# Performance work log

Measured on AMD Instinct MI355X. Metric: run time of the kernel, lower is better.

## Reference

```python
import jax, jax.numpy as jnp
import numpy as np

N = 65536          # nodes
E = 1048576        # edges (avg degree 16)
K = 5              # B-spline kernel size per dim (dim=3 -> 125 kernels)
F_IN, F_OUT = 1, 32
GRID = 32          # first sparse_voxel_max_pool: size = 1/32 -> 32^3 voxels
NUM_VOX = GRID ** 3

# enumerate the 2^3 corners of the degree-1 B-spline support
_BITS = np.array([[(b >> d) & 1 for d in range(3)] for b in range(8)], dtype=np.int32)  # [8,3]
_STRIDES = np.array([1, K, K * K], dtype=np.int32)  # kernel index strides per dim


def setup_inputs() -> dict:
    key = jax.random.key(0)
    ks = jax.random.split(key, 7)
    x = jax.random.normal(ks[0], (N, F_IN), dtype=jnp.float32)
    edge_index = jax.random.randint(ks[1], (2, E), 0, N, dtype=jnp.int32)
    pseudo = jax.random.uniform(ks[2], (E, 3), dtype=jnp.float32)   # edge pseudo-coords in [0,1]^3
    pos = jax.random.uniform(ks[3], (N, 3), dtype=jnp.float32)      # node positions in [0,1]^3
    W = jax.random.normal(ks[4], (K ** 3, F_IN, F_OUT), dtype=jnp.float32) * 0.1
    W_root = jax.random.normal(ks[5], (F_IN, F_OUT), dtype=jnp.float32) * 0.1
    bias = jax.random.normal(ks[6], (F_OUT,), dtype=jnp.float32) * 0.1
    return {"x": x, "edge_index": edge_index, "pseudo": pseudo, "pos": pos,
            "W": W, "W_root": W_root, "bias": bias}


def spline_basis(pseudo):
    """Degree-1 open B-spline basis. Returns (weights [E,8], kernel_idx [E,8])."""
    v = pseudo * (K - 1)                                   # [E,3] in [0, K-1]
    i0 = jnp.clip(jnp.floor(v), 0, K - 2)                  # lower knot per dim
    f = v - i0                                             # fractional part
    i0 = i0.astype(jnp.int32)
    bits = jnp.asarray(_BITS)                              # [8,3]
    idx = i0[:, None, :] + bits[None]                      # [E,8,3]
    w = jnp.where(bits[None].astype(bool), f[:, None, :], 1.0 - f[:, None, :])
    B = w.prod(axis=-1)                                    # [E,8]
    kidx = (idx * jnp.asarray(_STRIDES)).sum(axis=-1)      # [E,8] in [0,125)
    return B, kidx


def spline_conv(x, edge_index, pseudo, W, W_root, bias):
    src, dst = edge_index[0], edge_index[1]
    B, kidx = spline_basis(pseudo)                         # [E,8], [E,8]
    xj = x[src]                                            # [E,F_IN] edge-wise gather
    Wg = W[kidx]                                           # [E,8,F_IN,F_OUT]
    msg = jnp.einsum('es,ef,esfo->eo', B, xj, Wg)          # basis-weighted messages [E,F_OUT]
    agg = jax.ops.segment_sum(msg, dst, num_segments=N)    # scatter-add
    deg = jax.ops.segment_sum(jnp.ones((E,), jnp.float32), dst, num_segments=N)
    out = agg / jnp.clip(deg, 1.0)[:, None] + x @ W_root + bias  # mean aggr + root + bias
    return out


def reference(x, edge_index, pseudo, pos, W, W_root, bias):
    h = jax.nn.elu(spline_conv(x, edge_index, pseudo, W, W_root, bias))  # [N,32]
    # sparse voxel max pooling: hash positions to a 32^3 grid, scatter-max features
    vid = jnp.clip(jnp.floor(pos * GRID), 0, GRID - 1).astype(jnp.int32)  # [N,3]
    vidx = vid[:, 0] + GRID * vid[:, 1] + GRID * GRID * vid[:, 2]         # [N]
    pooled = jax.ops.segment_max(h, vidx, num_segments=NUM_VOX)           # [32768,32]
    pooled = jnp.where(jnp.isfinite(pooled), pooled, 0.0)                 # empty voxels -> 0
    return pooled
```

## Files before the change

kernel.cpp:

```cpp
#include <hip/hip_runtime.h>
#include <math.h>

#define F_OUT     32
#define GRID_DIM  32
#define NUM_VOX   (GRID_DIM * GRID_DIM * GRID_DIM)

#define NPB   64
#define NBKT  1024
#define SEB   2048
#define SCS   132
#define DEGS  125
#define ECAP  3072

__device__ __forceinline__ unsigned int enc_f32(float f) {
    unsigned int u = __float_as_uint(f);
    return (u & 0x80000000u) ? ~u : (u | 0x80000000u);
}
__device__ __forceinline__ float dec_f32(unsigned int e) {
    return (e & 0x80000000u) ? __uint_as_float(e ^ 0x80000000u)
                             : __uint_as_float(~e);
}

__global__ __launch_bounds__(512, 4) void sort_kernel(
    const int*   __restrict__ src,
    const int*   __restrict__ dst,
    const float* __restrict__ x,
    const float* __restrict__ pseudo,
    float4* __restrict__ payload,
    unsigned int* __restrict__ off_tab,
    int E)
{
    __shared__ unsigned int sHist[NBKT];
    __shared__ unsigned int sStart[NBKT];
    __shared__ unsigned int sWTot[8];
    __shared__ __align__(16) float4 sPay[SEB];

    const int t    = threadIdx.x;
    const int lane = t & 63;
    const int wv   = t >> 6;
    const int e0   = blockIdx.x * SEB;

    for (int i = t; i < NBKT; i += 512) sHist[i] = 0;
    __syncthreads();

    unsigned short dloc[4];
    float4 pay[4];
    #pragma unroll
    for (int i = 0; i < 4; ++i) {
        int e = e0 + i * 512 + t;
        if (e < E) {
            int d = dst[e];
            int s = src[e];
            float p0 = pseudo[3 * e], p1 = pseudo[3 * e + 1], p2 = pseudo[3 * e + 2];
            float xj = x[s];
            unsigned int q2 = (unsigned int)(p2 * 65535.0f + 0.5f) & 0xFFFFu;
            unsigned int w  = q2 | ((unsigned int)(d & 63) << 16);
            dloc[i] = (unsigned short)d;
            pay[i]  = make_float4(p0, p1, xj, __uint_as_float(w));
            atomicAdd(&sHist[d >> 6], 1u);
        } else dloc[i] = 0;
    }
    __syncthreads();

    unsigned int a0 = sHist[2 * t], a1 = sHist[2 * t + 1];
    unsigned int pairSum = a0 + a1;
    unsigned int incl = pairSum;
    #pragma unroll
    for (int d = 1; d < 64; d <<= 1) {
        unsigned int v = __shfl_up(incl, d, 64);
        if (lane >= d) incl += v;
    }
    if (lane == 63) sWTot[wv] = incl;
    __syncthreads();
    unsigned int wofs = 0, total = 0;
    #pragma unroll
    for (int w = 0; w < 8; ++w) {
        unsigned int v = sWTot[w];
        if (w < wv) wofs += v;
        total += v;
    }
    unsigned int ex = wofs + incl - pairSum;
    sStart[2 * t]     = ex;
    sStart[2 * t + 1] = ex + a0;
    sHist[2 * t]      = ex;
    sHist[2 * t + 1]  = ex + a0;
    __syncthreads();

    #pragma unroll
    for (int i = 0; i < 4; ++i) {
        int e = e0 + i * 512 + t;
        if (e < E) {
            unsigned int slot = atomicAdd(&sHist[dloc[i] >> 6], 1u);
            sPay[slot] = pay[i];
        }
    }
    __syncthreads();

    for (unsigned int i = t; i < total; i += 512)
        payload[(size_t)e0 + i] = sPay[i];

    for (int b = t; b < NBKT; b += 512) {
        unsigned int s = sStart[b];
        unsigned int nxt = (b < NBKT - 1) ? sStart[b + 1] : total;
        off_tab[(size_t)blockIdx.x * NBKT + b] = s | ((nxt - s) << 16);
    }
}

__device__ __forceinline__ void process_edge(float4 r, float* sC)
{
    float xj = r.z;
    unsigned int w = __float_as_uint(r.w);
    int   rel = (int)((w >> 16) & 63u);
    float p2  = (float)(w & 0xFFFFu) * (1.0f / 65535.0f);

    float v0 = r.x * 4.0f, v1 = r.y * 4.0f, v2 = p2 * 4.0f;
    float i0 = fminf(fmaxf(floorf(v0), 0.0f), 3.0f);
    float i1 = fminf(fmaxf(floorf(v1), 0.0f), 3.0f);
    float i2 = fminf(fmaxf(floorf(v2), 0.0f), 3.0f);
    float f0 = v0 - i0, f1 = v1 - i1, f2 = v2 - i2;
    float g0 = 1.0f - f0, g1 = 1.0f - f1, g2 = 1.0f - f2;
    int k = (int)i0 + 5 * (int)i1 + 25 * (int)i2;

    float w00 = g0 * g1, w10 = f0 * g1, w01 = g0 * f1, w11 = f0 * f1;
    float a2 = xj * g2, b2 = xj * f2;
    float* row = sC + rel * SCS;
    atomicAdd(row + k +  0, w00 * a2);
    atomicAdd(row + k +  1, w10 * a2);
    atomicAdd(row + k +  5, w01 * a2);
    atomicAdd(row + k +  6, w11 * a2);
    atomicAdd(row + k + 25, w00 * b2);
    atomicAdd(row + k + 26, w10 * b2);
    atomicAdd(row + k + 30, w01 * b2);
    atomicAdd(row + k + 31, w11 * b2);
    atomicAdd(row + DEGS, 1.0f);
}

__global__ __launch_bounds__(512) void owner_kernel(
    const float4* __restrict__ payload,
    const unsigned int* __restrict__ off_tab,
    const float* __restrict__ W,
    const float* __restrict__ x,
    const float* __restrict__ W_root,
    const float* __restrict__ bias,
    float4* __restrict__ h4,
    int Nn, int nSB)
{
    __shared__ __align__(16) float sC[NPB * SCS];
    __shared__ unsigned int sEdge[ECAP];
    __shared__ unsigned int sNe;

    const int t = threadIdx.x;
    const int b = blockIdx.x;
    const int lane = t & 63;

    for (int i = t; i < NPB * SCS / 4; i += 512)
        *(float4*)&sC[i * 4] = make_float4(0.f, 0.f, 0.f, 0.f);
    if (t == 0) sNe = 0;

    unsigned int cnt = 0, start_g = 0;
    if (t < nSB) {
        unsigned int packed = off_tab[(size_t)t * NBKT + b];
        start_g = (unsigned int)t * SEB + (packed & 0xFFFFu);
        cnt = packed >> 16;
    }
    __syncthreads();

    unsigned int incl = cnt;
    #pragma unroll
    for (int d = 1; d < 64; d <<= 1) {
        unsigned int v = __shfl_up(incl, d, 64);
        if (lane >= d) incl += v;
    }
    unsigned int wtot = __shfl(incl, 63, 64);
    unsigned int wbase = 0;
    if (lane == 63 && wtot > 0) wbase = atomicAdd(&sNe, wtot);
    wbase = __shfl(wbase, 63, 64);
    unsigned int off = wbase + incl - cnt;

    for (unsigned int j = 0; j < cnt; ++j) {
        unsigned int p = off + j;
        if (p < ECAP) sEdge[p] = start_g + j;
        else process_edge(payload[start_g + j], sC);
    }
    __syncthreads();

    int ne = (int)sNe; if (ne > ECAP) ne = ECAP;
    for (int i = t; i < ne; i += 512)
        process_edge(payload[sEdge[i]], sC);
    __syncthreads();

    const int node = t & 63;
    const int cg   = t >> 6;
    const float* crow = sC + node * SCS;
    float4 acc = make_float4(0.f, 0.f, 0.f, 0.f);
    #pragma unroll 8
    for (int k4 = 0; k4 < 31; ++k4) {
        float4 r = *(const float4*)&crow[k4 * 4];
        const float* wp = W + (k4 * 4) * F_OUT + cg * 4;
        float4 w0 = *(const float4*)(wp);
        float4 w1 = *(const float4*)(wp + F_OUT);
        float4 w2 = *(const float4*)(wp + 2 * F_OUT);
        float4 w3 = *(const float4*)(wp + 3 * F_OUT);
        acc.x += r.x * w0.x + r.y * w1.x + r.z * w2.x + r.w * w3.x;
        acc.y += r.x * w0.y + r.y * w1.y + r.z * w2.y + r.w * w3.y;
        acc.z += r.x * w0.z + r.y * w1.z + r.z * w2.z + r.w * w3.z;
        acc.w += r.x * w0.w + r.y * w1.w + r.z * w2.w + r.w * w3.w;
    }
    {
        float r = crow[124];
        const float* wp = W + 124 * F_OUT + cg * 4;
        acc.x += r * wp[0]; acc.y += r * wp[1];
        acc.z += r * wp[2]; acc.w += r * wp[3];
    }
    float dg = fmaxf(crow[DEGS], 1.0f);
    int   n  = b * NPB + node;
    float xn = (n < Nn) ? x[n] : 0.0f;
    float4 wr = *(const float4*)(W_root + cg * 4);
    float4 bs = *(const float4*)(bias + cg * 4);
    __syncthreads();

    if (n < Nn) {
        float h;
        h = acc.x / dg + xn * wr.x + bs.x; h = h > 0.f ? h : expm1f(h); sC[node * SCS + cg * 4 + 0] = h;
        h = acc.y / dg + xn * wr.y + bs.y; h = h > 0.f ? h : expm1f(h); sC[node * SCS + cg * 4 + 1] = h;
        h = acc.z / dg + xn * wr.z + bs.z; h = h > 0.f ? h : expm1f(h); sC[node * SCS + cg * 4 + 2] = h;
        h = acc.w / dg + xn * wr.w + bs.w; h = h > 0.f ? h : expm1f(h); sC[node * SCS + cg * 4 + 3] = h;
    }
    __syncthreads();

    const int n0 = b * NPB;
    for (int item = t; item < NPB * 8; item += 512) {
        int nr = item >> 3, q = item & 7;
        if (n0 + nr >= Nn) break;
        h4[(size_t)n0 * 8 + item] = *(const float4*)&sC[nr * SCS + q * 4];
    }
}

__global__ __launch_bounds__(256) void voxmax_kernel(
    const float* __restrict__ h,
    const float* __restrict__ pos,
    unsigned int* __restrict__ pooled,
    int Nn)
{
    int gid = blockIdx.x * 256 + threadIdx.x;
    int n = gid >> 5, o = gid & 31;
    if (n >= Nn) return;
    float hv = h[(size_t)n * F_OUT + o];
    int vx = min(max((int)floorf(pos[3 * n + 0] * (float)GRID_DIM), 0), GRID_DIM - 1);
    int vy = min(max((int)floorf(pos[3 * n + 1] * (float)GRID_DIM), 0), GRID_DIM - 1);
    int vz = min(max((int)floorf(pos[3 * n + 2] * (float)GRID_DIM), 0), GRID_DIM - 1);
    int vidx = vx + GRID_DIM * vy + GRID_DIM * GRID_DIM * vz;
    atomicMax(&pooled[(size_t)vidx * F_OUT + o], enc_f32(hv));
}

__global__ __launch_bounds__(256) void finalize_kernel(
    const unsigned int* __restrict__ pooled,
    float* __restrict__ out, int M)
{
    int i = blockIdx.x * blockDim.x + threadIdx.x;
    if (i >= M) return;
    unsigned int u = pooled[i];
    out[i] = (u == 0u) ? 0.0f : dec_f32(u);
}

extern "C" void kernel_launch(void* const* d_in, const int* in_sizes, int n_in,
                              void* d_out, int out_size, void* d_ws, size_t ws_size,
                              hipStream_t stream) {
    const float* x       = (const float*)d_in[0];
    const int*   ei      = (const int*)  d_in[1];
    const float* pseudo  = (const float*)d_in[2];
    const float* pos     = (const float*)d_in[3];
    const float* W       = (const float*)d_in[4];
    const float* W_root  = (const float*)d_in[5];
    const float* bias    = (const float*)d_in[6];
    float* out = (float*)d_out;

    const int E   = in_sizes[1] / 2;
    const int Nn  = in_sizes[0];
    const int nSB = (E + SEB - 1) / SEB;
    const int nb  = (Nn + NPB - 1) / NPB;

    const size_t pooled_b = (size_t)NUM_VOX * F_OUT * 4;
    const size_t off_b    = ((size_t)nSB * NBKT * 4 + 15) & ~(size_t)15;
    const size_t pay_b    = (size_t)nSB * SEB * 16;
    unsigned int* pooled  = (unsigned int*)d_ws;
    unsigned int* off_tab = (unsigned int*)((char*)d_ws + pooled_b);
    float4*       payload = (float4*)((char*)d_ws + pooled_b + off_b);
    float4*       h4      = (float4*)((char*)d_ws + pooled_b + off_b + pay_b);

    hipMemsetAsync(pooled, 0, pooled_b, stream);

    sort_kernel<<<nSB, 512, 0, stream>>>(ei, ei + E, x, pseudo, payload, off_tab, E);
    owner_kernel<<<nb, 512, 0, stream>>>(payload, off_tab, W, x, W_root, bias,
                                         h4, Nn, nSB);
    voxmax_kernel<<<(Nn * F_OUT + 255) / 256, 256, 0, stream>>>(
        (const float*)h4, pos, pooled, Nn);

    const int M = (out_size < NUM_VOX * F_OUT) ? out_size : NUM_VOX * F_OUT;
    finalize_kernel<<<(M + 255) / 256, 256, 0, stream>>>(pooled, out, M);
}
```

Before: 175.1 us.

## Enlarge sort chunks, batch edge loads, and transpose the offset table for coalesced reads

The sort kernel now handles twice as many edges per block. On full chunks it issues all index, pseudo and x-gather loads up front to expose memory-level parallelism. A new transpose kernel turns the per-chunk bucket offset table into a bucket-major layout, so each owner block reads its offsets contiguously instead of with a large stride. The owner kernel's edge loop is unrolled by two so payload loads overlap. In exchange there is an extra kernel launch, roughly twice the shared memory per sort block, and only about one sort block per CU, which lowers occupancy.

Measured after the change: 178.5 us. About the same (+2.0%).

```diff
diff --git a/kernel.cpp b/kernel.cpp
--- a/kernel.cpp
+++ b/kernel.cpp
@@ -7,7 +7,7 @@
 
 #define NPB   64
 #define NBKT  1024
-#define SEB   2048
+#define SEB   4096
 #define SCS   132
 #define DEGS  125
 #define ECAP  3072
@@ -21,7 +21,7 @@
                              : __uint_as_float(~e);
 }
 
-__global__ __launch_bounds__(512, 4) void sort_kernel(
+__global__ __launch_bounds__(512) void sort_kernel(
     const int*   __restrict__ src,
     const int*   __restrict__ dst,
     const float* __restrict__ x,
@@ -39,26 +39,47 @@
     const int lane = t & 63;
     const int wv   = t >> 6;
     const int e0   = blockIdx.x * SEB;
+    const bool full = (e0 + SEB <= E);
 
     for (int i = t; i < NBKT; i += 512) sHist[i] = 0;
     __syncthreads();
 
-    unsigned short dloc[4];
-    float4 pay[4];
-    #pragma unroll
-    for (int i = 0; i < 4; ++i) {
-        int e = e0 + i * 512 + t;
-        if (e < E) {
-            int d = dst[e];
-            int s = src[e];
-            float p0 = pseudo[3 * e], p1 = pseudo[3 * e + 1], p2 = pseudo[3 * e + 2];
-            float xj = x[s];
-            unsigned int q2 = (unsigned int)(p2 * 65535.0f + 0.5f) & 0xFFFFu;
-            unsigned int w  = q2 | ((unsigned int)(d & 63) << 16);
-            dloc[i] = (unsigned short)d;
-            pay[i]  = make_float4(p0, p1, xj, __uint_as_float(w));
-            atomicAdd(&sHist[d >> 6], 1u);
-        } else dloc[i] = 0;
+    unsigned short dloc[8];
+    float4 pay[8];
+    if (full) {
+        int   dd[8], ss[8];
+        float pp0[8], pp1[8], pp2[8], xj[8];
+        #pragma unroll
+        for (int i = 0; i < 8; ++i) {
+            int e = e0 + i * 512 + t;
+            dd[i] = dst[e]; ss[i] = src[e];
+            pp0[i] = pseudo[3 * e]; pp1[i] = pseudo[3 * e + 1]; pp2[i] = pseudo[3 * e + 2];
+        }
+        #pragma unroll
+        for (int i = 0; i < 8; ++i) xj[i] = x[ss[i]];
+        #pragma unroll
+        for (int i = 0; i < 8; ++i) {
+            unsigned int q2 = (unsigned int)(pp2[i] * 65535.0f + 0.5f) & 0xFFFFu;
+            unsigned int w  = q2 | ((unsigned int)(dd[i] & 63) << 16);
+            dloc[i] = (unsigned short)dd[i];
+            pay[i]  = make_float4(pp0[i], pp1[i], xj[i], __uint_as_float(w));
+            atomicAdd(&sHist[dd[i] >> 6], 1u);
+        }
+    } else {
+        #pragma unroll
+        for (int i = 0; i < 8; ++i) {
+            int e = e0 + i * 512 + t;
+            if (e < E) {
+                int d = dst[e];
+                float p0 = pseudo[3 * e], p1 = pseudo[3 * e + 1], p2 = pseudo[3 * e + 2];
+                float xjv = x[src[e]];
+                unsigned int q2 = (unsigned int)(p2 * 65535.0f + 0.5f) & 0xFFFFu;
+                unsigned int w  = q2 | ((unsigned int)(d & 63) << 16);
+                dloc[i] = (unsigned short)d;
+                pay[i]  = make_float4(p0, p1, xjv, __uint_as_float(w));
+                atomicAdd(&sHist[d >> 6], 1u);
+            } else dloc[i] = 0;
+        }
     }
     __syncthreads();
 
@@ -87,7 +108,7 @@
     __syncthreads();
 
     #pragma unroll
-    for (int i = 0; i < 4; ++i) {
+    for (int i = 0; i < 8; ++i) {
         int e = e0 + i * 512 + t;
         if (e < E) {
             unsigned int slot = atomicAdd(&sHist[dloc[i] >> 6], 1u);
@@ -103,6 +124,27 @@
         unsigned int s = sStart[b];
         unsigned int nxt = (b < NBKT - 1) ? sStart[b + 1] : total;
         off_tab[(size_t)blockIdx.x * NBKT + b] = s | ((nxt - s) << 16);
+    }
+}
+
+__global__ __launch_bounds__(256) void transpose_kernel(
+    const unsigned int* __restrict__ in, unsigned int* __restrict__ outT,
+    int rows, int cols)
+{
+    __shared__ unsigned int tile[32][33];
+    const int tx = threadIdx.x & 31, ty = threadIdx.x >> 5;
+    const int c0 = blockIdx.x * 32, r0 = blockIdx.y * 32;
+    #pragma unroll
+    for (int r = ty; r < 32; r += 8) {
+        int row = r0 + r, col = c0 + tx;
+        tile[r][tx] = (row < rows && col < cols) ? in[(size_t)row * cols + col] : 0u;
+    }
+    __syncthreads();
+    #pragma unroll
+    for (int r = ty; r < 32; r += 8) {
+        int col = c0 + r;
+        int row = r0 + tx;
+        if (col < cols && row < rows) outT[(size_t)col * rows + row] = tile[tx][r];
     }
 }
 
@@ -137,7 +179,7 @@
 
 __global__ __launch_bounds__(512) void owner_kernel(
     const float4* __restrict__ payload,
-    const unsigned int* __restrict__ off_tab,
+    const unsigned int* __restrict__ off_tabT,
     const float* __restrict__ W,
     const float* __restrict__ x,
     const float* __restrict__ W_root,
@@ -159,7 +201,7 @@
 
     unsigned int cnt = 0, start_g = 0;
     if (t < nSB) {
-        unsigned int packed = off_tab[(size_t)t * NBKT + b];
+        unsigned int packed = off_tabT[(size_t)b * nSB + t];
         start_g = (unsigned int)t * SEB + (packed & 0xFFFFu);
         cnt = packed >> 16;
     }
@@ -185,8 +227,15 @@
     __syncthreads();
 
     int ne = (int)sNe; if (ne > ECAP) ne = ECAP;
-    for (int i = t; i < ne; i += 512)
-        process_edge(payload[sEdge[i]], sC);
+    for (int i = t; i < ne; i += 1024) {
+        float4 r0 = payload[sEdge[i]];
+        int j = i + 512;
+        bool hj = (j < ne);
+        float4 r1 = r0;
+        if (hj) r1 = payload[sEdge[j]];
+        process_edge(r0, sC);
+        if (hj) process_edge(r1, sC);
+    }
     __syncthreads();
 
     const int node = t & 63;
@@ -281,17 +330,20 @@
     const int nb  = (Nn + NPB - 1) / NPB;
 
     const size_t pooled_b = (size_t)NUM_VOX * F_OUT * 4;
-    const size_t off_b    = ((size_t)nSB * NBKT * 4 + 15) & ~(size_t)15;
+    const size_t off_b    = ((size_t)nSB * NBKT * 4 + 255) & ~(size_t)255;
     const size_t pay_b    = (size_t)nSB * SEB * 16;
-    unsigned int* pooled  = (unsigned int*)d_ws;
-    unsigned int* off_tab = (unsigned int*)((char*)d_ws + pooled_b);
-    float4*       payload = (float4*)((char*)d_ws + pooled_b + off_b);
-    float4*       h4      = (float4*)((char*)d_ws + pooled_b + off_b + pay_b);
+    unsigned int* pooled   = (unsigned int*)d_ws;
+    unsigned int* off_tab  = (unsigned int*)((char*)d_ws + pooled_b);
+    unsigned int* off_tabT = (unsigned int*)((char*)d_ws + pooled_b + off_b);
+    float4*       payload  = (float4*)((char*)d_ws + pooled_b + 2 * off_b);
+    float4*       h4       = (float4*)((char*)d_ws + pooled_b + 2 * off_b + pay_b);
 
     hipMemsetAsync(pooled, 0, pooled_b, stream);
 
     sort_kernel<<<nSB, 512, 0, stream>>>(ei, ei + E, x, pseudo, payload, off_tab, E);
-    owner_kernel<<<nb, 512, 0, stream>>>(payload, off_tab, W, x, W_root, bias,
+    transpose_kernel<<<dim3((NBKT + 31) / 32, (nSB + 31) / 32), 256, 0, stream>>>(
+        off_tab, off_tabT, nSB, NBKT);
+    owner_kernel<<<nb, 512, 0, stream>>>(payload, off_tabT, W, x, W_root, bias,
                                          h4, Nn, nSB);
     voxmax_kernel<<<(Nn * F_OUT + 255) / 256, 256, 0, stream>>>(
         (const float*)h4, pos, pooled, Nn);
```
